# Kernel optimization log

Hardware: AMD Instinct MI355X
Metric: run time of the kernel (lower is better)

Reference implementation:

```python
import jax, jax.numpy as jnp
import numpy as np

N_NODES = 100000
N_EDGES = 1600000
D_IN = 128
D_HID = 128


def setup_inputs() -> dict:
    key = jax.random.key(0)
    ks = jax.random.split(key, 8)
    s_in = 1.0 / np.sqrt(D_IN)
    s_h = 1.0 / np.sqrt(D_HID)
    return {
        "x": jax.random.normal(ks[0], (N_NODES, D_IN), dtype=jnp.float32),
        "edge_index": jax.random.randint(ks[1], (2, N_EDGES), 0, N_NODES, dtype=jnp.int32),
        "edge_weight": jax.random.uniform(ks[2], (N_EDGES,), dtype=jnp.float32),
        "W0l": jax.random.normal(ks[3], (D_IN, D_HID), dtype=jnp.float32) * s_in,
        "b0l": jnp.zeros((D_HID,), dtype=jnp.float32),
        "W0r": jax.random.normal(ks[4], (D_IN, D_HID), dtype=jnp.float32) * s_in,
        "W2l": jax.random.normal(ks[5], (D_HID, D_HID), dtype=jnp.float32) * s_h,
        "b2l": jnp.zeros((D_HID,), dtype=jnp.float32),
        "W2r": jax.random.normal(ks[6], (D_HID, D_HID), dtype=jnp.float32) * s_h,
    }


def _sage_conv(x, src, dst, Wl, bl, Wr):
    # PyG SAGEConv: mean-aggregate source features onto targets, then
    # out = lin_l(aggr) + lin_r(x)   (bias only on lin_l)
    msgs = x[src]  # [E, D] gather
    summed = jax.ops.segment_sum(msgs, dst, num_segments=N_NODES)  # [N, D]
    deg = jax.ops.segment_sum(jnp.ones((src.shape[0],), x.dtype), dst,
                              num_segments=N_NODES)
    mean = summed / jnp.maximum(deg, 1.0)[:, None]
    return mean @ Wl + bl + x @ Wr


def reference(x, edge_index, edge_weight, W0l, b0l, W0r, W2l, b2l, W2r):
    src, dst = edge_index[0], edge_index[1]
    # layer 0 (the only layer hit by `for i in range(num_layers-2)`)
    h = jax.nn.relu(_sage_conv(x, src, dst, W0l, b0l, W0r))
    mid_node_feats = [h]
    # layer num_layers-1 (layer 1 is constructed but never called in forward)
    fea = jax.nn.relu(_sage_conv(h, src, dst, W2l, b2l, W2r))
    # dropout is identity at inference (training=False)
    return (fea, *mid_node_feats)
```

## Files before the change

kernel.cpp:

```cpp
#include <hip/hip_runtime.h>
#include <hip/hip_bf16.h>

#define N_NODES 100000
#define N_EDGES 1600000
#define D 128
#define NF (N_NODES * D)

#define NGROUPS 8
#define NODES_PER_GROUP ((N_NODES + NGROUPS - 1) / NGROUPS)
#define EPB 4096

__global__ __launch_bounds__(256) void deg_count_part_kernel(
    const int* __restrict__ dst, int* __restrict__ deg, int nE) {
    const int g = blockIdx.x & (NGROUPS - 1);
    const int chunk = blockIdx.x >> 3;
    const int base = chunk * EPB;
    const unsigned lo = (unsigned)(g * NODES_PER_GROUP);
    for (int i = threadIdx.x; i < EPB; i += 256) {
        int e = base + i;
        if (e >= nE) break;
        int d = dst[e];
        if ((unsigned)(d - lo) < (unsigned)NODES_PER_GROUP) {
            atomicAdd(&deg[d], 1);
        }
    }
}

__global__ __launch_bounds__(1024) void scan1_kernel(
    const int* __restrict__ deg, int* __restrict__ rowptr,
    int* __restrict__ bsums, int n) {
    __shared__ int buf[1024];
    int i = blockIdx.x * 1024 + threadIdx.x;
    int v = (i < n) ? deg[i] : 0;
    buf[threadIdx.x] = v;
    __syncthreads();
    for (int off = 1; off < 1024; off <<= 1) {
        int t = (threadIdx.x >= off) ? buf[threadIdx.x - off] : 0;
        __syncthreads();
        if (threadIdx.x >= off) buf[threadIdx.x] += t;
        __syncthreads();
    }
    if (i < n) rowptr[i] = buf[threadIdx.x] - v;
    if (threadIdx.x == 1023) bsums[blockIdx.x] = buf[1023];
}

__global__ __launch_bounds__(128) void scan2_kernel(int* __restrict__ bsums,
                                                    int nb) {
    __shared__ int buf[128];
    int v = (threadIdx.x < nb) ? bsums[threadIdx.x] : 0;
    buf[threadIdx.x] = v;
    __syncthreads();
    for (int off = 1; off < 128; off <<= 1) {
        int t = (threadIdx.x >= off) ? buf[threadIdx.x - off] : 0;
        __syncthreads();
        if (threadIdx.x >= off) buf[threadIdx.x] += t;
        __syncthreads();
    }
    if (threadIdx.x < nb) bsums[threadIdx.x] = buf[threadIdx.x] - v;
}

__global__ __launch_bounds__(1024) void scan3_kernel(
    int* __restrict__ rowptr, const int* __restrict__ bsums,
    int* __restrict__ cursor, int n, int nE) {
    int i = blockIdx.x * 1024 + threadIdx.x;
    if (i < n) {
        int r = rowptr[i] + bsums[blockIdx.x];
        rowptr[i] = r;
        cursor[i] = r;
    }
    if (i == 0) rowptr[n] = nE;
}

__global__ __launch_bounds__(256) void csr_fill_part_kernel(
    const int* __restrict__ src,
    const int* __restrict__ dst,
    int* __restrict__ cursor,
    int* __restrict__ col, int nE) {
    const int g = blockIdx.x & (NGROUPS - 1);
    const int chunk = blockIdx.x >> 3;
    const int base = chunk * EPB;
    const unsigned lo = (unsigned)(g * NODES_PER_GROUP);
    for (int i = threadIdx.x; i < EPB; i += 256) {
        int e = base + i;
        if (e >= nE) break;
        int d = dst[e];
        if ((unsigned)(d - lo) < (unsigned)NODES_PER_GROUP) {
            int p = atomicAdd(&cursor[d], 1);
            col[p] = src[e];
        }
    }
}

__global__ __launch_bounds__(256) void aggregate_mean_kernel(
    const float* __restrict__ X,
    const int* __restrict__ rowptr,
    const int* __restrict__ col,
    float* __restrict__ mean) {
    int node = (int)((blockIdx.x * blockDim.x + threadIdx.x) >> 6);
    int lane = threadIdx.x & 63;
    if (node >= N_NODES) return;
    int beg = rowptr[node];
    int end = rowptr[node + 1];
    float a0x = 0.f, a0y = 0.f, a1x = 0.f, a1y = 0.f;
    int p = beg;
    for (; p + 3 < end; p += 4) {
        int s0 = col[p];
        int s1 = col[p + 1];
        int s2 = col[p + 2];
        int s3 = col[p + 3];
        float2 v0 = ((const float2*)(X + (size_t)s0 * D))[lane];
        float2 v1 = ((const float2*)(X + (size_t)s1 * D))[lane];
        float2 v2 = ((const float2*)(X + (size_t)s2 * D))[lane];
        float2 v3 = ((const float2*)(X + (size_t)s3 * D))[lane];
        a0x += v0.x + v1.x;
        a0y += v0.y + v1.y;
        a1x += v2.x + v3.x;
        a1y += v2.y + v3.y;
    }
    for (; p < end; ++p) {
        int s = col[p];
        float2 v = ((const float2*)(X + (size_t)s * D))[lane];
        a0x += v.x;
        a0y += v.y;
    }
    int dg = end - beg;
    float invd = 1.0f / (float)(dg > 1 ? dg : 1);
    float2 o;
    o.x = (a0x + a1x) * invd;
    o.y = (a0y + a1y) * invd;
    ((float2*)(mean + (size_t)node * D))[lane] = o;
}

#define BM 128
#define BK 32

__global__ __launch_bounds__(256) void sage_gemm_kernel(
    const float* __restrict__ Amean,
    const float* __restrict__ Aself,
    const float* __restrict__ Wl,
    const float* __restrict__ Wr,
    const float* __restrict__ bias,
    float* __restrict__ Out,
    int nrows) {
    __shared__ float As[BM][BK + 4];
    __shared__ float Bs[BK][132];

    const int tid = threadIdx.x;
    const int row0 = blockIdx.x * BM;
    const int tx = tid & 15;
    const int ty = tid >> 4;

    float acc[8][8];
#pragma unroll
    for (int i = 0; i < 8; i++)
#pragma unroll
        for (int j = 0; j < 8; j++) acc[i][j] = 0.f;

    for (int step = 0; step < 8; ++step) {
        const int k0 = step * BK;
        const float* A = (k0 < 128) ? Amean : Aself;
        const float* W = (k0 < 128) ? Wl : Wr;
        const int kc = k0 & 127;

        {
            int r = tid >> 1;
            int kk0 = (tid & 1) * 16;
            int gr = row0 + r;
            if (gr >= nrows) gr = nrows - 1;
            const float4* srcp = (const float4*)(A + (size_t)gr * D + kc + kk0);
#pragma unroll
            for (int q = 0; q < 4; q++) {
                float4 v = srcp[q];
                *(float4*)&As[r][kk0 + 4 * q] = v;
            }
        }
        {
            int kk = tid >> 3;
            int c = tid & 7;
            const float4* srcp = (const float4*)(W + (size_t)(kc + kk) * D);
#pragma unroll
            for (int q = 0; q < 4; q++) {
                float4 v = srcp[c + 8 * q];
                *(float4*)&Bs[kk][(c + 8 * q) * 4] = v;
            }
        }
        __syncthreads();

#pragma unroll
        for (int kk = 0; kk < BK; ++kk) {
            float a[8], b[8];
#pragma unroll
            for (int i = 0; i < 8; i++) a[i] = As[ty * 8 + i][kk];
            float4 b0 = *(const float4*)&Bs[kk][tx * 4];
            float4 b1 = *(const float4*)&Bs[kk][64 + tx * 4];
            b[0] = b0.x; b[1] = b0.y; b[2] = b0.z; b[3] = b0.w;
            b[4] = b1.x; b[5] = b1.y; b[6] = b1.z; b[7] = b1.w;
#pragma unroll
            for (int i = 0; i < 8; i++)
#pragma unroll
                for (int j = 0; j < 8; j++) acc[i][j] += a[i] * b[j];
        }
        __syncthreads();
    }

    float4 bv0 = *(const float4*)&bias[tx * 4];
    float4 bv1 = *(const float4*)&bias[64 + tx * 4];
#pragma unroll
    for (int i = 0; i < 8; i++) {
        int gr = row0 + ty * 8 + i;
        if (gr < nrows) {
            float4 o0, o1;
            o0.x = fmaxf(acc[i][0] + bv0.x, 0.f);
            o0.y = fmaxf(acc[i][1] + bv0.y, 0.f);
            o0.z = fmaxf(acc[i][2] + bv0.z, 0.f);
            o0.w = fmaxf(acc[i][3] + bv0.w, 0.f);
            o1.x = fmaxf(acc[i][4] + bv1.x, 0.f);
            o1.y = fmaxf(acc[i][5] + bv1.y, 0.f);
            o1.z = fmaxf(acc[i][6] + bv1.z, 0.f);
            o1.w = fmaxf(acc[i][7] + bv1.w, 0.f);
            *(float4*)(Out + (size_t)gr * D + tx * 4) = o0;
            *(float4*)(Out + (size_t)gr * D + 64 + tx * 4) = o1;
        }
    }
}

extern "C" void kernel_launch(void* const* d_in, const int* in_sizes, int n_in,
                              void* d_out, int out_size, void* d_ws,
                              size_t ws_size, hipStream_t stream) {
    const float* x   = (const float*)d_in[0];
    const int*   ei  = (const int*)d_in[1];
    const float* W0l = (const float*)d_in[3];
    const float* b0l = (const float*)d_in[4];
    const float* W0r = (const float*)d_in[5];
    const float* W2l = (const float*)d_in[6];
    const float* b2l = (const float*)d_in[7];
    const float* W2r = (const float*)d_in[8];

    const int* src = ei;
    const int* dst = ei + N_EDGES;

    float* fea = (float*)d_out;
    float* h   = (float*)d_out + NF;
    float* meanbuf = fea;

    char* ws = (char*)d_ws;
    int* deg    = (int*)ws;
    int* rowptr = (int*)(ws + 400000);
    int* bsums  = (int*)(ws + 800032);
    int* cursor = (int*)(ws + 800544);
    int* col    = (int*)(ws + 1200544);

    const int nScanBlocks = (N_NODES + 1023) / 1024;
    const int nChunks = (N_EDGES + EPB - 1) / EPB;

    hipMemsetAsync(deg, 0, N_NODES * sizeof(int), stream);
    deg_count_part_kernel<<<nChunks * NGROUPS, 256, 0, stream>>>(dst, deg,
                                                                 N_EDGES);
    scan1_kernel<<<nScanBlocks, 1024, 0, stream>>>(deg, rowptr, bsums, N_NODES);
    scan2_kernel<<<1, 128, 0, stream>>>(bsums, nScanBlocks);
    scan3_kernel<<<nScanBlocks, 1024, 0, stream>>>(rowptr, bsums, cursor,
                                                   N_NODES, N_EDGES);
    csr_fill_part_kernel<<<nChunks * NGROUPS, 256, 0, stream>>>(src, dst,
                                                                cursor, col,
                                                                N_EDGES);

    const int aggGrid = (N_NODES * 64 + 255) / 256;
    const int gemmGrid = (N_NODES + BM - 1) / BM;

    aggregate_mean_kernel<<<aggGrid, 256, 0, stream>>>(x, rowptr, col, meanbuf);
    sage_gemm_kernel<<<gemmGrid, 256, 0, stream>>>(meanbuf, x, W0l, W0r, b0l, h,
                                                   N_NODES);

    aggregate_mean_kernel<<<aggGrid, 256, 0, stream>>>(h, rowptr, col, meanbuf);
    sage_gemm_kernel<<<gemmGrid, 256, 0, stream>>>(meanbuf, h, W2l, W2r, b2l,
                                                   fea, N_NODES);
}
```

Measured before the change: 714.7 us.

## Gather neighbor features from bf16 copies in mean aggregation

```diff
diff --git a/kernel.cpp b/kernel.cpp
--- a/kernel.cpp
+++ b/kernel.cpp
@@ -9,6 +9,27 @@
 #define NGROUPS 8
 #define NODES_PER_GROUP ((N_NODES + NGROUPS - 1) / NGROUPS)
 #define EPB 4096
+
+static __device__ __forceinline__ unsigned short f32_to_bf16_rne(float f) {
+    unsigned u = __float_as_uint(f);
+    unsigned lsb = (u >> 16) & 1u;
+    u += 0x7fffu + lsb;
+    return (unsigned short)(u >> 16);
+}
+
+__global__ __launch_bounds__(256) void convert_bf16_kernel(
+    const float* __restrict__ in, unsigned* __restrict__ out, int n8) {
+    int i = blockIdx.x * blockDim.x + threadIdx.x;
+    if (i >= n8) return;
+    const float4* p = (const float4*)(in + (size_t)i * 8);
+    float4 a = p[0], b = p[1];
+    uint4 o;
+    o.x = (unsigned)f32_to_bf16_rne(a.x) | ((unsigned)f32_to_bf16_rne(a.y) << 16);
+    o.y = (unsigned)f32_to_bf16_rne(a.z) | ((unsigned)f32_to_bf16_rne(a.w) << 16);
+    o.z = (unsigned)f32_to_bf16_rne(b.x) | ((unsigned)f32_to_bf16_rne(b.y) << 16);
+    o.w = (unsigned)f32_to_bf16_rne(b.z) | ((unsigned)f32_to_bf16_rne(b.w) << 16);
+    ((uint4*)out)[i] = o;
+}
 
 __global__ __launch_bounds__(256) void deg_count_part_kernel(
     const int* __restrict__ dst, int* __restrict__ deg, int nE) {
@@ -89,6 +110,46 @@
             col[p] = src[e];
         }
     }
+}
+
+__global__ __launch_bounds__(256) void aggregate_mean_bf16_kernel(
+    const unsigned short* __restrict__ Xb,
+    const int* __restrict__ rowptr,
+    const int* __restrict__ col,
+    float* __restrict__ mean) {
+    int node = (int)((blockIdx.x * blockDim.x + threadIdx.x) >> 6);
+    int lane = threadIdx.x & 63;
+    if (node >= N_NODES) return;
+    int beg = rowptr[node];
+    int end = rowptr[node + 1];
+    float a0x = 0.f, a0y = 0.f, a1x = 0.f, a1y = 0.f;
+    int p = beg;
+    for (; p + 3 < end; p += 4) {
+        int s0 = col[p];
+        int s1 = col[p + 1];
+        int s2 = col[p + 2];
+        int s3 = col[p + 3];
+        unsigned v0 = ((const unsigned*)(Xb + (size_t)s0 * D))[lane];
+        unsigned v1 = ((const unsigned*)(Xb + (size_t)s1 * D))[lane];
+        unsigned v2 = ((const unsigned*)(Xb + (size_t)s2 * D))[lane];
+        unsigned v3 = ((const unsigned*)(Xb + (size_t)s3 * D))[lane];
+        a0x += __uint_as_float(v0 << 16) + __uint_as_float(v1 << 16);
+        a0y += __uint_as_float(v0 & 0xffff0000u) + __uint_as_float(v1 & 0xffff0000u);
+        a1x += __uint_as_float(v2 << 16) + __uint_as_float(v3 << 16);
+        a1y += __uint_as_float(v2 & 0xffff0000u) + __uint_as_float(v3 & 0xffff0000u);
+    }
+    for (; p < end; ++p) {
+        int s = col[p];
+        unsigned v = ((const unsigned*)(Xb + (size_t)s * D))[lane];
+        a0x += __uint_as_float(v << 16);
+        a0y += __uint_as_float(v & 0xffff0000u);
+    }
+    int dg = end - beg;
+    float invd = 1.0f / (float)(dg > 1 ? dg : 1);
+    float2 o;
+    o.x = (a0x + a1x) * invd;
+    o.y = (a0y + a1y) * invd;
+    ((float2*)(mean + (size_t)node * D))[lane] = o;
 }
 
 __global__ __launch_bounds__(256) void aggregate_mean_kernel(
@@ -141,6 +202,7 @@
     const float* __restrict__ Wr,
     const float* __restrict__ bias,
     float* __restrict__ Out,
+    unsigned short* __restrict__ OutBf,
     int nrows) {
     __shared__ float As[BM][BK + 4];
     __shared__ float Bs[BK][132];
@@ -220,6 +282,19 @@
             o1.w = fmaxf(acc[i][7] + bv1.w, 0.f);
             *(float4*)(Out + (size_t)gr * D + tx * 4) = o0;
             *(float4*)(Out + (size_t)gr * D + 64 + tx * 4) = o1;
+            if (OutBf) {
+                uint2 p0, p1;
+                p0.x = (unsigned)f32_to_bf16_rne(o0.x) |
+                       ((unsigned)f32_to_bf16_rne(o0.y) << 16);
+                p0.y = (unsigned)f32_to_bf16_rne(o0.z) |
+                       ((unsigned)f32_to_bf16_rne(o0.w) << 16);
+                p1.x = (unsigned)f32_to_bf16_rne(o1.x) |
+                       ((unsigned)f32_to_bf16_rne(o1.y) << 16);
+                p1.y = (unsigned)f32_to_bf16_rne(o1.z) |
+                       ((unsigned)f32_to_bf16_rne(o1.w) << 16);
+                *(uint2*)(OutBf + (size_t)gr * D + tx * 4) = p0;
+                *(uint2*)(OutBf + (size_t)gr * D + 64 + tx * 4) = p1;
+            }
         }
     }
 }
@@ -249,6 +324,8 @@
     int* bsums  = (int*)(ws + 800032);
     int* cursor = (int*)(ws + 800544);
     int* col    = (int*)(ws + 1200544);
+    unsigned short* xb = (unsigned short*)(ws + 7600640);
+    const bool use_bf16 = (ws_size >= (size_t)33200640);
 
     const int nScanBlocks = (N_NODES + 1023) / 1024;
     const int nChunks = (N_EDGES + EPB - 1) / EPB;
@@ -267,11 +344,30 @@
     const int aggGrid = (N_NODES * 64 + 255) / 256;
     const int gemmGrid = (N_NODES + BM - 1) / BM;
 
-    aggregate_mean_kernel<<<aggGrid, 256, 0, stream>>>(x, rowptr, col, meanbuf);
-    sage_gemm_kernel<<<gemmGrid, 256, 0, stream>>>(meanbuf, x, W0l, W0r, b0l, h,
-                                                   N_NODES);
-
-    aggregate_mean_kernel<<<aggGrid, 256, 0, stream>>>(h, rowptr, col, meanbuf);
-    sage_gemm_kernel<<<gemmGrid, 256, 0, stream>>>(meanbuf, h, W2l, W2r, b2l,
-                                                   fea, N_NODES);
-}
+    if (use_bf16) {
+        convert_bf16_kernel<<<(NF / 8 + 255) / 256, 256, 0, stream>>>(
+            x, (unsigned*)xb, NF / 8);
+
+        aggregate_mean_bf16_kernel<<<aggGrid, 256, 0, stream>>>(xb, rowptr,
+                                                                col, meanbuf);
+        sage_gemm_kernel<<<gemmGrid, 256, 0, stream>>>(meanbuf, x, W0l, W0r,
+                                                       b0l, h, xb, N_NODES);
+
+        aggregate_mean_bf16_kernel<<<aggGrid, 256, 0, stream>>>(xb, rowptr,
+                                                                col, meanbuf);
+        sage_gemm_kernel<<<gemmGrid, 256, 0, stream>>>(meanbuf, h, W2l, W2r,
+                                                       b2l, fea, (unsigned short*)nullptr,
+                                                       N_NODES);
+    } else {
+        aggregate_mean_kernel<<<aggGrid, 256, 0, stream>>>(x, rowptr, col,
+                                                           meanbuf);
+        sage_gemm_kernel<<<gemmGrid, 256, 0, stream>>>(meanbuf, x, W0l, W0r,
+                                                       b0l, h, (unsigned short*)nullptr,
+                                                       N_NODES);
+        aggregate_mean_kernel<<<aggGrid, 256, 0, stream>>>(h, rowptr, col,
+                                                           meanbuf);
+        sage_gemm_kernel<<<gemmGrid, 256, 0, stream>>>(meanbuf, h, W2l, W2r,
+                                                       b2l, fea, (unsigned short*)nullptr,
+                                                       N_NODES);
+    }
+}
```

After: 644.6 us. -9.8%, faster.
